# Kernel optimization log

Measured on AMD Instinct MI355X. Metric: run time of the kernel, lower is better.

The kernel has to match this reference:

```python
import jax, jax.numpy as jnp
import numpy as np

B = 4096      # graphs
N = 21        # nodes per graph (EEG electrodes)
CIN = 512
H1 = 1024
H2 = 1024
COUT = 512
R = 4         # SE reduction
RANK = 10     # nodevec rank
EPS = 1e-5
THRESH = 0.1


def setup_inputs() -> dict:
    key = jax.random.key(0)
    ks = jax.random.split(key, 16)
    p = lambda i, shape, s=0.02: (jax.random.normal(ks[i], shape, jnp.float32) * s)
    return {
        "x": jax.random.normal(ks[0], (B * N, CIN), jnp.float32),
        "batch": jnp.arange(B * N, dtype=jnp.int32) // N,
        "nodevec1": jax.random.normal(ks[1], (N, RANK), jnp.float32),
        "nodevec2": jax.random.normal(ks[2], (RANK, N), jnp.float32),
        "se_w1": p(3, (CIN, CIN // R), 0.05),
        "se_w2": p(4, (CIN // R, CIN), 0.05),
        "W1": p(5, (CIN, H1)), "b1": jnp.zeros((H1,), jnp.float32),
        "W2": p(6, (H1, H2)), "b2": jnp.zeros((H2,), jnp.float32),
        "W3": p(7, (H2, COUT)), "b3": jnp.zeros((COUT,), jnp.float32),
        "bn1_g": jnp.ones((H1,), jnp.float32), "bn1_b": jnp.zeros((H1,), jnp.float32),
        "bn2_g": jnp.ones((H2,), jnp.float32), "bn2_b": jnp.zeros((H2,), jnp.float32),
        "bn3_g": jnp.ones((COUT,), jnp.float32), "bn3_b": jnp.zeros((COUT,), jnp.float32),
        "rs1_w": p(8, (CIN, H1)), "rs1_b": jnp.zeros((H1,), jnp.float32),
        "fc_w": p(9, (COUT, 2 * COUT)), "fc_b": jnp.zeros((2 * COUT,), jnp.float32),
    }


def _batchnorm(h, g, b):
    # training-mode BN: biased batch stats over the node dimension
    m = h.mean(0)
    v = h.var(0)
    return (h - m) * jax.lax.rsqrt(v + EPS) * g + b


def _gcn(A, h, W, b):
    # GCNConv with precomputed normalized+thresholded weights:
    # out = A_block_diag @ (h @ W) + b, done densely per graph since A is 21x21
    hm = (h @ W).reshape(B, N, -1)                 # [B, N, Cout]
    agg = jnp.einsum('ij,bjc->bic', A, hm)         # message passing per graph
    return agg.reshape(B * N, -1) + b


def _forward(x, batch, nodevec1, nodevec2, se_w1, se_w2,
             W1, b1, W2, b2, W3, b3,
             bn1_g, bn1_b, bn2_g, bn2_b, bn3_g, bn3_b,
             rs1_w, rs1_b, fc_w, fc_b):
    # SE layer on [B, N, C]: channel-wise gating from node-mean features
    x3 = x.reshape(B, N, CIN)
    y = jax.nn.sigmoid(jax.nn.relu(x3.mean(1) @ se_w1) @ se_w2)   # [B, C]
    xg = (x3 * y[:, None, :]).reshape(B * N, CIN)
    # adaptive adjacency: sigmoid(nv1 @ nv2), symmetric normalize, threshold
    adp = jax.nn.sigmoid(nodevec1 @ nodevec2)                      # [N, N]
    at = adp + jnp.eye(N, dtype=adp.dtype)
    deg = at.sum(1)
    dinv = jnp.where(deg > 0, deg ** -0.5, 0.0)
    A = dinv[:, None] * at * dinv[None, :]
    A = jnp.where(A > THRESH, A, 0.0)
    # layer 1 (+ projected residual, BN, relu; dropout omitted = eval)
    h = _batchnorm(_gcn(A, xg, W1, b1), bn1_g, bn1_b) + (xg @ rs1_w + rs1_b)
    h = jax.nn.relu(h)
    # layer 2 (h1 == h2 -> identity residual)
    h = jax.nn.relu(_batchnorm(_gcn(A, h, W2, b2), bn2_g, bn2_b) + h)
    # layer 3
    h = _batchnorm(_gcn(A, h, W3, b3), bn3_g, bn3_b)
    # global mean pool by graph id
    ssum = jax.ops.segment_sum(h, batch, num_segments=B)
    cnt = jax.ops.segment_sum(jnp.ones((h.shape[0], 1), h.dtype), batch, num_segments=B)
    pooled = ssum / cnt
    return pooled @ fc_w + fc_b                                    # [B, 2*COUT]


def reference(x, batch, nodevec1, nodevec2, se_w1, se_w2,
              W1, b1, W2, b2, W3, b3,
              bn1_g, bn1_b, bn2_g, bn2_b, bn3_g, bn3_b,
              rs1_w, rs1_b, fc_w, fc_b):
    return _forward(x, batch, nodevec1, nodevec2, se_w1, se_w2,
                    W1, b1, W2, b2, W3, b3,
                    bn1_g, bn1_b, bn2_g, bn2_b, bn3_g, bn3_b,
                    rs1_w, rs1_b, fc_w, fc_b)
```

## Files before the change

### kernel.cpp

```cpp
#include <hip/hip_runtime.h>

typedef _Float16 f16;
typedef f16 f16x2 __attribute__((ext_vector_type(2)));
typedef f16 f16x8 __attribute__((ext_vector_type(8)));
typedef float f32x4 __attribute__((ext_vector_type(4)));
typedef const void __attribute__((address_space(1)))* gas1;
typedef void __attribute__((address_space(3)))* las3;

#define NB 4096
#define NN 21
#define MROWS (NB*NN)
#define CIN 512

__global__ void k_adj(const float* __restrict__ nv1, const float* __restrict__ nv2,
                      float* __restrict__ Aout) {
  __shared__ float at[21][21];
  __shared__ float dinv[21];
  int t = threadIdx.x;
  if (t < 441) {
    int i = t / 21, j = t % 21;
    float s = 0.f;
    #pragma unroll
    for (int r = 0; r < 10; r++) s += nv1[i*10 + r] * nv2[r*21 + j];
    float v = 1.f / (1.f + expf(-s));
    if (i == j) v += 1.f;
    at[i][j] = v;
  }
  __syncthreads();
  if (t < 21) {
    float d = 0.f;
    #pragma unroll
    for (int j = 0; j < 21; j++) d += at[t][j];
    dinv[t] = d > 0.f ? rsqrtf(d) : 0.f;
  }
  __syncthreads();
  if (t < 441) {
    int i = t / 21, j = t % 21;
    float a = dinv[i] * at[i][j] * dinv[j];
    Aout[t] = a > 0.1f ? a : 0.f;
  }
}

__global__ void k_transpose(const float* __restrict__ src, f16* __restrict__ dst,
                            int K, int N) {
  __shared__ float tile[32][33];
  int n0 = blockIdx.x * 32, k0 = blockIdx.y * 32;
  int tx = threadIdx.x, ty = threadIdx.y;
  #pragma unroll
  for (int i = 0; i < 4; i++)
    tile[ty + 8*i][tx] = src[(size_t)(k0 + ty + 8*i) * N + n0 + tx];
  __syncthreads();
  #pragma unroll
  for (int i = 0; i < 4; i++)
    dst[(size_t)(n0 + ty + 8*i) * K + k0 + tx] = (f16)tile[tx][ty + 8*i];
}

__global__ void k_mean(const float* __restrict__ x, float* __restrict__ xm) {
  int b = blockIdx.x, t = threadIdx.x;
  for (int c = t; c < CIN; c += 256) {
    float s = 0.f;
    #pragma unroll
    for (int n = 0; n < NN; n++) s += x[((size_t)b*NN + n)*CIN + c];
    xm[(size_t)b*CIN + c] = s * (1.f/21.f);
  }
}

__global__ void k_se1(const float* __restrict__ xm, const float* __restrict__ w1,
                      float* __restrict__ y1) {
  __shared__ float row[CIN];
  int b = blockIdx.x, t = threadIdx.x;
  for (int k = t; k < CIN; k += 128) row[k] = xm[(size_t)b*CIN + k];
  __syncthreads();
  float acc = 0.f;
  for (int k = 0; k < CIN; k++) acc += row[k] * w1[(size_t)k*128 + t];
  y1[(size_t)b*128 + t] = fmaxf(acc, 0.f);
}

__global__ void k_se2(const float* __restrict__ y1, const float* __restrict__ w2,
                      float* __restrict__ y) {
  __shared__ float row[128];
  int b = blockIdx.x, t = threadIdx.x;
  if (t < 128) row[t] = y1[(size_t)b*128 + t];
  __syncthreads();
  float acc = 0.f;
  for (int k = 0; k < 128; k++) acc += row[k] * w2[(size_t)k*CIN + t];
  y[(size_t)b*CIN + t] = 1.f / (1.f + expf(-acc));
}

__global__ void k_gate(const float* __restrict__ x, const float* __restrict__ y,
                       f16* __restrict__ xg) {
  size_t i8 = (size_t)blockIdx.x * 256 + threadIdx.x;
  size_t base = i8 * 8;
  int r = (int)(base >> 9);
  int c = (int)(base & 511);
  int b = r / 21;
  const float4* xp = (const float4*)(x + base);
  const float4* yp = (const float4*)(y + (size_t)b*CIN + c);
  float4 a0 = xp[0], a1 = xp[1];
  float4 g0 = yp[0], g1 = yp[1];
  f16x8 o;
  o[0] = (f16)(a0.x * g0.x); o[1] = (f16)(a0.y * g0.y);
  o[2] = (f16)(a0.z * g0.z); o[3] = (f16)(a0.w * g0.w);
  o[4] = (f16)(a1.x * g1.x); o[5] = (f16)(a1.y * g1.y);
  o[6] = (f16)(a1.z * g1.z); o[7] = (f16)(a1.w * g1.w);
  *(f16x8*)(xg + base) = o;
}

#define GBM 128
#define GBN 128
#define HBUF 32768

template<int MODE>
__global__ __launch_bounds__(256, 2)
void k_gemm4(const f16* __restrict__ A, const f16* __restrict__ BT,
             f16* __restrict__ C1, const float* __restrict__ bias,
             float* __restrict__ Cf, float* __restrict__ psum,
             float* __restrict__ psq, int N, int K, int lgn) {
  __shared__ __align__(16) char lds[2 * HBUF];
  const int tid = threadIdx.x;
  const int nwg = gridDim.x;
  const int g = blockIdx.x;
  const int swz = (g & 7) * (nwg >> 3) + (g >> 3);
  const int bn = swz & ((1 << lgn) - 1);
  const int bm = swz >> lgn;
  const int lane = tid & 63;
  const int wid = tid >> 6;
  const int wr = wid >> 1;
  const int wc = wid & 1;
  const int fr = lane & 15;
  const int kg = lane >> 4;

  size_t srcOff[8]; int ldsOff[8];
  #pragma unroll
  for (int j = 0; j < 8; j++) {
    int gid = j * 256 + tid;
    int row = (gid >> 3) & 127;
    int gr = gid & 7;
    int gsw = gr ^ (row & 7);
    if (gid < 1024) {
      srcOff[j] = (size_t)(bm * GBM + row) * K + gsw * 8;
      ldsOff[j] = gid * 16;
    } else {
      srcOff[j] = (size_t)(bn * GBN + row) * K + gsw * 8;
      ldsOff[j] = 16384 + (gid - 1024) * 16;
    }
  }

  int aOff[4], axor[4], bOff[4], bxor[4];
  #pragma unroll
  for (int m = 0; m < 4; m++) {
    int row = wr*64 + m*16 + fr;
    aOff[m] = row * 128; axor[m] = row & 7;
  }
  #pragma unroll
  for (int n = 0; n < 4; n++) {
    int row = wc*64 + n*16 + fr;
    bOff[n] = 16384 + row * 128; bxor[n] = row & 7;
  }

  f32x4 acc[4][4];
  #pragma unroll
  for (int m = 0; m < 4; m++)
    #pragma unroll
    for (int n = 0; n < 4; n++)
      #pragma unroll
      for (int r = 0; r < 4; r++) acc[m][n][r] = 0.f;

  auto STAGE8 = [&](int t2, int sbuf) {
    char* dst = (char*)lds + sbuf * HBUF;
    const size_t kof = (size_t)t2 * 64;
    #pragma unroll
    for (int j = 0; j < 8; j++) {
      const f16* src = (j < 4 ? A : BT) + srcOff[j] + kof;
      __builtin_amdgcn_global_load_lds((gas1)src, (las3)(dst + ldsOff[j]), 16, 0, 0);
    }
  };
  auto READF = [&](f16x8* avv, f16x8* bvv, const char* rb, int s) {
    #pragma unroll
    for (int m = 0; m < 4; m++)
      avv[m] = *(const f16x8*)(rb + aOff[m] + (((s*4 + kg) ^ axor[m]) << 4));
    #pragma unroll
    for (int n = 0; n < 4; n++)
      bvv[n] = *(const f16x8*)(rb + bOff[n] + (((s*4 + kg) ^ bxor[n]) << 4));
  };

  f16x8 av0[4], bv0[4], av1[4], bv1[4];
  const int NT = K >> 6;
  STAGE8(0, 0);
  asm volatile("s_waitcnt vmcnt(0)" ::: "memory");
  asm volatile("s_barrier" ::: "memory");
  READF(av0, bv0, (const char*)lds, 0);

  for (int t = 0; t < NT; t++) {
    const char* rb  = (const char*)lds + (t & 1) * HBUF;
    const char* rbn = (const char*)lds + ((t + 1) & 1) * HBUF;
    const bool stg = (t + 1) < NT;

    if (stg) STAGE8(t + 1, (t + 1) & 1);
    READF(av1, bv1, rb, 1);
    __builtin_amdgcn_s_setprio(1);
    #pragma unroll
    for (int m = 0; m < 4; m++)
      #pragma unroll
      for (int n = 0; n < 4; n++)
        acc[m][n] = __builtin_amdgcn_mfma_f32_16x16x32_f16(av0[m], bv0[n], acc[m][n], 0, 0, 0);
    __builtin_amdgcn_s_setprio(0);
    if (stg) asm volatile("s_waitcnt vmcnt(0)" ::: "memory");
    asm volatile("s_barrier" ::: "memory");
    if (stg) READF(av0, bv0, rbn, 0);
    __builtin_amdgcn_s_setprio(1);
    #pragma unroll
    for (int m = 0; m < 4; m++)
      #pragma unroll
      for (int n = 0; n < 4; n++)
        acc[m][n] = __builtin_amdgcn_mfma_f32_16x16x32_f16(av1[m], bv1[n], acc[m][n], 0, 0, 0);
    __builtin_amdgcn_s_setprio(0);
  }

  const int crow = bm * GBM + wr * 64 + ((lane >> 4) << 2);
  const int ccol = bn * GBN + wc * 64 + fr;
  if constexpr (MODE == 2) {
    #pragma unroll
    for (int n = 0; n < 4; n++) {
      float bb = bias[ccol + n*16];
      #pragma unroll
      for (int m = 0; m < 4; m++)
        #pragma unroll
        for (int r = 0; r < 4; r++)
          Cf[(size_t)(crow + m*16 + r) * N + (ccol + n*16)] = acc[m][n][r] + bb;
    }
  } else {
    #pragma unroll
    for (int m = 0; m < 4; m++)
      #pragma unroll
      for (int n = 0; n < 4; n++)
        #pragma unroll
        for (int r = 0; r < 4; r++)
          C1[(size_t)(crow + m*16 + r) * N + (ccol + n*16)] = (f16)acc[m][n][r];
  }
  if constexpr (MODE == 1) {
    float s[4], q[4];
    #pragma unroll
    for (int n = 0; n < 4; n++) {
      float ss = 0.f, qq = 0.f;
      #pragma unroll
      for (int m = 0; m < 4; m++)
        #pragma unroll
        for (int r = 0; r < 4; r++) { float v = acc[m][n][r]; ss += v; qq = fmaf(v, v, qq); }
      s[n] = ss; q[n] = qq;
    }
    #pragma unroll
    for (int n = 0; n < 4; n++) {
      s[n] += __shfl_xor(s[n], 16); s[n] += __shfl_xor(s[n], 32);
      q[n] += __shfl_xor(q[n], 16); q[n] += __shfl_xor(q[n], 32);
    }
    float* wred = (float*)lds;
    __syncthreads();
    if ((lane >> 4) == 0) {
      #pragma unroll
      for (int n = 0; n < 4; n++) {
        wred[wr*128 + wc*64 + n*16 + fr]       = s[n];
        wred[256 + wr*128 + wc*64 + n*16 + fr] = q[n];
      }
    }
    __syncthreads();
    if (tid < 128) {
      psum[(size_t)bm * N + bn*128 + tid] = wred[tid]       + wred[128 + tid];
      psq [(size_t)bm * N + bn*128 + tid] = wred[256 + tid] + wred[384 + tid];
    }
  }
}

__global__ __launch_bounds__(256)
void k_mixip(f16* __restrict__ t, const float* __restrict__ Aadj) {
  __shared__ float A[441];
  int b = blockIdx.x, tid = threadIdx.x;
  for (int i = tid; i < 441; i += 256) A[i] = Aadj[i];
  __syncthreads();
  int c0 = tid * 2;
  size_t base = (size_t)b * NN * 512 + c0;
  float vx[21], vy[21];
  #pragma unroll
  for (int j = 0; j < 21; j++) {
    f16x2 v = *(const f16x2*)(t + base + (size_t)j * 512);
    vx[j] = (float)v[0]; vy[j] = (float)v[1];
  }
  #pragma unroll
  for (int i = 0; i < 21; i++) {
    float a0 = 0.f, a1 = 0.f;
    #pragma unroll
    for (int j = 0; j < 21; j++) { float w = A[i*21+j]; a0 = fmaf(w, vx[j], a0); a1 = fmaf(w, vy[j], a1); }
    f16x2 o; o[0] = (f16)a0; o[1] = (f16)a1;
    *(f16x2*)(t + base + (size_t)i * 512) = o;
  }
}

__global__ __launch_bounds__(256)
void k_mix(f16* __restrict__ t, const float* __restrict__ Aadj,
           float* __restrict__ psum, float* __restrict__ psq, int C) {
  __shared__ float A[441];
  int b = blockIdx.x, tid = threadIdx.x;
  for (int i = tid; i < 441; i += 256) A[i] = Aadj[i];
  __syncthreads();
  int c0 = (blockIdx.y * 256 + tid) * 2;
  size_t base = (size_t)b * NN * C + c0;
  float vx[21], vy[21];
  #pragma unroll
  for (int j = 0; j < 21; j++) {
    f16x2 v = *(const f16x2*)(t + base + (size_t)j * C);
    vx[j] = (float)v[0]; vy[j] = (float)v[1];
  }
  float s0 = 0.f, s1 = 0.f, q0 = 0.f, q1 = 0.f;
  #pragma unroll
  for (int i = 0; i < 21; i++) {
    float a0 = 0.f, a1 = 0.f;
    #pragma unroll
    for (int j = 0; j < 21; j++) {
      float w = A[i*21 + j];
      a0 = fmaf(w, vx[j], a0);
      a1 = fmaf(w, vy[j], a1);
    }
    f16x2 o; o[0] = (f16)a0; o[1] = (f16)a1;
    *(f16x2*)(t + base + (size_t)i * C) = o;
    s0 += a0; s1 += a1;
    q0 = fmaf(a0, a0, q0); q1 = fmaf(a1, a1, q1);
  }
  float2 sv; sv.x = s0; sv.y = s1;
  float2 qv; qv.x = q0; qv.y = q1;
  *(float2*)(psum + (size_t)b * C + c0) = sv;
  *(float2*)(psq  + (size_t)b * C + c0) = qv;
}

__global__ void k_reduce(const float* __restrict__ ps, const float* __restrict__ pq,
                         float* __restrict__ rs, float* __restrict__ rq,
                         int C, int per) {
  int c = blockIdx.x * 256 + threadIdx.x;
  int py = blockIdx.y;
  float s = 0.f, q = 0.f;
  for (int p = py*per; p < py*per + per; p++) {
    s += ps[(size_t)p*C + c];
    q += pq[(size_t)p*C + c];
  }
  rs[(size_t)py*C + c] = s;
  rq[(size_t)py*C + c] = q;
}

__global__ void k_bnparams(const float* __restrict__ psum, const float* __restrict__ psq,
                           const float* __restrict__ gamma, const float* __restrict__ beta,
                           const float* __restrict__ resbias,
                           float* __restrict__ scale, float* __restrict__ shift,
                           int C, int npart) {
  int c = blockIdx.x * 256 + threadIdx.x;
  float s = 0.f, q = 0.f;
  for (int p = 0; p < npart; p++) { s += psum[(size_t)p*C + c]; q += psq[(size_t)p*C + c]; }
  const float Minv = 1.f / (float)MROWS;
  float mean = s * Minv;
  float var = q * Minv - mean * mean;
  float sc = gamma[c] * rsqrtf(var + 1e-5f);
  float sh = beta[c] - mean * sc;
  if (resbias) sh += resbias[c];
  scale[c] = sc; shift[c] = sh;
}

__global__ void k_finalize(const f16* __restrict__ g, const f16* res,
                           f16* dst, const float* __restrict__ scale,
                           const float* __restrict__ shift, int cmask) {
  size_t i8 = (size_t)blockIdx.x * 256 + threadIdx.x;
  size_t base = i8 * 8;
  int c = (int)(base & (size_t)cmask);
  f16x8 gv = *(const f16x8*)(g + base);
  f16x8 rv = *(const f16x8*)(res + base);
  f16x8 o;
  #pragma unroll
  for (int j = 0; j < 8; j++) {
    float v = (float)gv[j] * scale[c + j] + shift[c + j] + (float)rv[j];
    o[j] = (f16)fmaxf(v, 0.f);
  }
  *(f16x8*)(dst + base) = o;
}

__global__ __launch_bounds__(256)
void k_finmix(const f16* t, const f16* res, f16* hout, f16* hmix,
              const float* __restrict__ scale, const float* __restrict__ shift,
              const float* __restrict__ Aadj, int C) {
  __shared__ float A[441];
  int b = blockIdx.x, tid = threadIdx.x;
  for (int i = tid; i < 441; i += 256) A[i] = Aadj[i];
  __syncthreads();
  int c0 = (blockIdx.y * 256 + tid) * 2;
  float scx = scale[c0], scy = scale[c0+1];
  float shx = shift[c0], shy = shift[c0+1];
  size_t base = (size_t)b * NN * C + c0;
  float hx[21], hy[21];
  #pragma unroll
  for (int j = 0; j < 21; j++) {
    f16x2 tv = *(const f16x2*)(t + base + (size_t)j*C);
    f16x2 rv = *(const f16x2*)(res + base + (size_t)j*C);
    hx[j] = fmaxf((float)tv[0]*scx + shx + (float)rv[0], 0.f);
    hy[j] = fmaxf((float)tv[1]*scy + shy + (float)rv[1], 0.f);
    if (hout) {
      f16x2 o; o[0] = (f16)hx[j]; o[1] = (f16)hy[j];
      *(f16x2*)(hout + base + (size_t)j*C) = o;
    }
  }
  #pragma unroll
  for (int i = 0; i < 21; i++) {
    float a0 = 0.f, a1 = 0.f;
    #pragma unroll
    for (int j = 0; j < 21; j++) { float w = A[i*21+j]; a0 = fmaf(w, hx[j], a0); a1 = fmaf(w, hy[j], a1); }
    f16x2 o; o[0] = (f16)a0; o[1] = (f16)a1;
    *(f16x2*)(hmix + base + (size_t)i*C) = o;
  }
}

__global__ void k_pool(const f16* __restrict__ g3, const float* __restrict__ scale,
                       const float* __restrict__ shift, f16* __restrict__ pooled) {
  int b = blockIdx.x, t = threadIdx.x;
  for (int c = t; c < 512; c += 256) {
    float s = 0.f;
    #pragma unroll
    for (int n = 0; n < NN; n++) s += (float)g3[((size_t)b*NN + n)*512 + c];
    pooled[(size_t)b*512 + c] = (f16)((s * (1.f/21.f)) * scale[c] + shift[c]);
  }
}

extern "C" void kernel_launch(void* const* d_in, const int* in_sizes, int n_in,
                              void* d_out, int out_size, void* d_ws, size_t ws_size,
                              hipStream_t stream) {
  const float* x     = (const float*)d_in[0];
  const float* nv1   = (const float*)d_in[2];
  const float* nv2   = (const float*)d_in[3];
  const float* se_w1 = (const float*)d_in[4];
  const float* se_w2 = (const float*)d_in[5];
  const float* W1    = (const float*)d_in[6];
  const float* W2    = (const float*)d_in[8];
  const float* W3    = (const float*)d_in[10];
  const float* bn1g  = (const float*)d_in[12];
  const float* bn1b  = (const float*)d_in[13];
  const float* bn2g  = (const float*)d_in[14];
  const float* bn2b  = (const float*)d_in[15];
  const float* bn3g  = (const float*)d_in[16];
  const float* bn3b  = (const float*)d_in[17];
  const float* rs1w  = (const float*)d_in[18];
  const float* rs1b  = (const float*)d_in[19];
  const float* fcw   = (const float*)d_in[20];
  const float* fcb   = (const float*)d_in[21];
  float* out = (float*)d_out;

  char* ws = (char*)d_ws;
  size_t off = 0;
  auto alloc = [&](size_t bytes) -> char* {
    char* p = ws + off;
    off = (off + bytes + 255) & ~(size_t)255;
    return p;
  };

  float* A_adj = (float*)alloc(441 * 4);
  f16* W1T  = (f16*)alloc((size_t)1024 * 512 * 2);
  f16* RS1T = (f16*)alloc((size_t)1024 * 512 * 2);
  f16* W2T  = (f16*)alloc((size_t)1024 * 1024 * 2);
  f16* W3T  = (f16*)alloc((size_t)512 * 1024 * 2);
  f16* FCWT = (f16*)alloc((size_t)1024 * 512 * 2);
  float* psum = (float*)alloc((size_t)NB * 1024 * 4);
  float* psq  = (float*)alloc((size_t)NB * 1024 * 4);
  float* y1   = (float*)alloc((size_t)NB * 128 * 4);
  float* rsum = (float*)alloc((size_t)32 * 1024 * 4);
  float* rsq  = (float*)alloc((size_t)32 * 1024 * 4);
  float* sc1 = (float*)alloc(1024 * 4);
  float* sh1 = (float*)alloc(1024 * 4);
  float* sc2 = (float*)alloc(1024 * 4);
  float* sh2 = (float*)alloc(1024 * 4);
  float* sc3 = (float*)alloc(1024 * 4);
  float* sh3 = (float*)alloc(1024 * 4);
  f16* pooled = (f16*)alloc((size_t)NB * 512 * 2);
  f16* G = (f16*)alloc((size_t)MROWS * 512 * 2);
  f16* R = (f16*)alloc((size_t)MROWS * 1024 * 2);
  f16* T = (f16*)alloc((size_t)MROWS * 1024 * 2);
  float* xm = psum;
  float* yv = psq;
  (void)ws_size; (void)in_sizes; (void)n_in; (void)out_size;

  k_adj<<<1, 512, 0, stream>>>(nv1, nv2, A_adj);
  k_transpose<<<dim3(32, 16), dim3(32, 8), 0, stream>>>(W1,   W1T,  512, 1024);
  k_transpose<<<dim3(32, 16), dim3(32, 8), 0, stream>>>(rs1w, RS1T, 512, 1024);
  k_transpose<<<dim3(32, 32), dim3(32, 8), 0, stream>>>(W2,   W2T,  1024, 1024);
  k_transpose<<<dim3(16, 32), dim3(32, 8), 0, stream>>>(W3,   W3T,  1024, 512);
  k_transpose<<<dim3(32, 16), dim3(32, 8), 0, stream>>>(fcw,  FCWT, 512, 1024);

  k_mean<<<NB, 256, 0, stream>>>(x, xm);
  k_se1<<<NB, 128, 0, stream>>>(xm, se_w1, y1);
  k_se2<<<NB, 512, 0, stream>>>(y1, se_w2, yv);
  k_gate<<<21504, 256, 0, stream>>>(x, yv, G);

  k_gemm4<0><<<672*8, 256, 0, stream>>>(G, RS1T, R, nullptr, nullptr, nullptr, nullptr, 1024, 512, 3);
  k_mixip<<<NB, 256, 0, stream>>>(G, A_adj);
  k_gemm4<1><<<672*8, 256, 0, stream>>>(G, W1T, T, nullptr, nullptr, psum, psq, 1024, 512, 3);
  k_reduce<<<dim3(4, 32), 256, 0, stream>>>(psum, psq, rsum, rsq, 1024, 21);
  k_bnparams<<<4, 256, 0, stream>>>(rsum, rsq, bn1g, bn1b, rs1b, sc1, sh1, 1024, 32);
  k_finalize<<<43008, 256, 0, stream>>>(T, R, R, sc1, sh1, 1023);

  k_gemm4<0><<<672*8, 256, 0, stream>>>(R, W2T, T, nullptr, nullptr, nullptr, nullptr, 1024, 1024, 3);
  k_mix<<<dim3(NB, 2), 256, 0, stream>>>(T, A_adj, psum, psq, 1024);
  k_reduce<<<dim3(4, 32), 256, 0, stream>>>(psum, psq, rsum, rsq, 1024, 128);
  k_bnparams<<<4, 256, 0, stream>>>(rsum, rsq, bn2g, bn2b, nullptr, sc2, sh2, 1024, 32);
  k_finmix<<<dim3(NB, 2), 256, 0, stream>>>(T, R, nullptr, T, sc2, sh2, A_adj, 1024);

  k_gemm4<1><<<672*4, 256, 0, stream>>>(T, W3T, G, nullptr, nullptr, psum, psq, 512, 1024, 2);
  k_reduce<<<dim3(2, 32), 256, 0, stream>>>(psum, psq, rsum, rsq, 512, 21);
  k_bnparams<<<2, 256, 0, stream>>>(rsum, rsq, bn3g, bn3b, nullptr, sc3, sh3, 512, 32);

  k_pool<<<NB, 256, 0, stream>>>(G, sc3, sh3, pooled);
  k_gemm4<2><<<32*8, 256, 0, stream>>>(pooled, FCWT, nullptr, fcb, out, nullptr, nullptr, 1024, 512, 3);
}
```

Before: 1.214 ms.

## Switch GEMMs to 256x256 tiles with 512 threads and vectorized epilogue

Replaces the 128x128, 256-thread GEMM with a 256x256, 512-thread (8-wave) kernel using 128 KB of double-buffered LDS. Global-to-LDS staging is split into halves interleaved with the two MFMA sub-steps, and operands are swapped so each lane owns four contiguous output columns, allowing f16x4 and float4 stores. The goals are higher arithmetic intensity per LDS byte, fewer global loads per FLOP and wider stores. In exchange, occupancy drops to one workgroup per CU and register pressure rises. The BN partial-sum layout and the reduce/bnparams launch counts change to match the new row-block count.

```diff
diff --git a/kernel.cpp b/kernel.cpp
--- a/kernel.cpp
+++ b/kernel.cpp
@@ -2,6 +2,7 @@
 
 typedef _Float16 f16;
 typedef f16 f16x2 __attribute__((ext_vector_type(2)));
+typedef f16 f16x4 __attribute__((ext_vector_type(4)));
 typedef f16 f16x8 __attribute__((ext_vector_type(8)));
 typedef float f32x4 __attribute__((ext_vector_type(4)));
 typedef const void __attribute__((address_space(1)))* gas1;
@@ -106,17 +107,15 @@
   *(f16x8*)(xg + base) = o;
 }
 
-#define GBM 128
-#define GBN 128
-#define HBUF 32768
+#define QBUF 65536
 
 template<int MODE>
-__global__ __launch_bounds__(256, 2)
-void k_gemm4(const f16* __restrict__ A, const f16* __restrict__ BT,
-             f16* __restrict__ C1, const float* __restrict__ bias,
-             float* __restrict__ Cf, float* __restrict__ psum,
-             float* __restrict__ psq, int N, int K, int lgn) {
-  __shared__ __align__(16) char lds[2 * HBUF];
+__global__ __launch_bounds__(512, 1)
+void k_gemm256(const f16* __restrict__ A, const f16* __restrict__ BT,
+               f16* __restrict__ C1, const float* __restrict__ bias,
+               float* __restrict__ Cf, float* __restrict__ psum,
+               float* __restrict__ psq, int N, int K, int lgn) {
+  __shared__ __align__(16) char lds[2 * QBUF];
   const int tid = threadIdx.x;
   const int nwg = gridDim.x;
   const int g = blockIdx.x;
@@ -125,148 +124,145 @@
   const int bm = swz >> lgn;
   const int lane = tid & 63;
   const int wid = tid >> 6;
-  const int wr = wid >> 1;
-  const int wc = wid & 1;
+  const int wr = wid >> 2;
+  const int wc = wid & 3;
   const int fr = lane & 15;
   const int kg = lane >> 4;
 
-  size_t srcOff[8]; int ldsOff[8];
+  int srcOff[8];
   #pragma unroll
   for (int j = 0; j < 8; j++) {
-    int gid = j * 256 + tid;
-    int row = (gid >> 3) & 127;
+    int gid = j * 512 + tid;
+    int row = (gid >> 3) & 255;
     int gr = gid & 7;
     int gsw = gr ^ (row & 7);
-    if (gid < 1024) {
-      srcOff[j] = (size_t)(bm * GBM + row) * K + gsw * 8;
-      ldsOff[j] = gid * 16;
-    } else {
-      srcOff[j] = (size_t)(bn * GBN + row) * K + gsw * 8;
-      ldsOff[j] = 16384 + (gid - 1024) * 16;
-    }
-  }
-
-  int aOff[4], axor[4], bOff[4], bxor[4];
-  #pragma unroll
-  for (int m = 0; m < 4; m++) {
-    int row = wr*64 + m*16 + fr;
-    aOff[m] = row * 128; axor[m] = row & 7;
-  }
-  #pragma unroll
-  for (int n = 0; n < 4; n++) {
-    int row = wc*64 + n*16 + fr;
-    bOff[n] = 16384 + row * 128; bxor[n] = row & 7;
-  }
-
-  f32x4 acc[4][4];
-  #pragma unroll
-  for (int m = 0; m < 4; m++)
+    srcOff[j] = ((j < 4 ? bm : bn) * 256 + row) * K + gsw * 8;
+  }
+  const int ldsBase = tid * 16;
+
+  const int x7 = fr & 7;
+  const int aBase = (wr*128 + fr) * 128;
+  const int bBase = 32768 + (wc*64 + fr) * 128;
+
+  f32x4 acc[8][4];
+  #pragma unroll
+  for (int m = 0; m < 8; m++)
     #pragma unroll
     for (int n = 0; n < 4; n++)
       #pragma unroll
       for (int r = 0; r < 4; r++) acc[m][n][r] = 0.f;
 
-  auto STAGE8 = [&](int t2, int sbuf) {
-    char* dst = (char*)lds + sbuf * HBUF;
+  auto STAGEH = [&](int t2, int sbuf, int j0) {
+    char* dst = (char*)lds + sbuf * QBUF;
     const size_t kof = (size_t)t2 * 64;
     #pragma unroll
-    for (int j = 0; j < 8; j++) {
+    for (int j = j0; j < j0 + 2; j++) {
       const f16* src = (j < 4 ? A : BT) + srcOff[j] + kof;
-      __builtin_amdgcn_global_load_lds((gas1)src, (las3)(dst + ldsOff[j]), 16, 0, 0);
+      __builtin_amdgcn_global_load_lds((gas1)src, (las3)(dst + ldsBase + j*8192), 16, 0, 0);
     }
   };
-  auto READF = [&](f16x8* avv, f16x8* bvv, const char* rb, int s) {
-    #pragma unroll
-    for (int m = 0; m < 4; m++)
-      avv[m] = *(const f16x8*)(rb + aOff[m] + (((s*4 + kg) ^ axor[m]) << 4));
-    #pragma unroll
-    for (int n = 0; n < 4; n++)
-      bvv[n] = *(const f16x8*)(rb + bOff[n] + (((s*4 + kg) ^ bxor[n]) << 4));
+  auto READF = [&](f16x8* av, f16x8* bv, const char* rb, int s) {
+    const int ko = ((s*4 + kg) ^ x7) << 4;
+    #pragma unroll
+    for (int m = 0; m < 8; m++) av[m] = *(const f16x8*)(rb + aBase + m*2048 + ko);
+    #pragma unroll
+    for (int n = 0; n < 4; n++) bv[n] = *(const f16x8*)(rb + bBase + n*2048 + ko);
   };
 
-  f16x8 av0[4], bv0[4], av1[4], bv1[4];
+  f16x8 av[8], bv[4];
   const int NT = K >> 6;
-  STAGE8(0, 0);
+  STAGEH(0, 0, 0); STAGEH(0, 0, 2); STAGEH(0, 0, 4); STAGEH(0, 0, 6);
   asm volatile("s_waitcnt vmcnt(0)" ::: "memory");
   asm volatile("s_barrier" ::: "memory");
-  READF(av0, bv0, (const char*)lds, 0);
 
   for (int t = 0; t < NT; t++) {
-    const char* rb  = (const char*)lds + (t & 1) * HBUF;
-    const char* rbn = (const char*)lds + ((t + 1) & 1) * HBUF;
+    const char* rb = (const char*)lds + (t & 1) * QBUF;
+    const int nb = (t + 1) & 1;
     const bool stg = (t + 1) < NT;
 
-    if (stg) STAGE8(t + 1, (t + 1) & 1);
-    READF(av1, bv1, rb, 1);
+    if (stg) { STAGEH(t + 1, nb, 0); STAGEH(t + 1, nb, 2); }
+    READF(av, bv, rb, 0);
     __builtin_amdgcn_s_setprio(1);
     #pragma unroll
-    for (int m = 0; m < 4; m++)
+    for (int m = 0; m < 8; m++)
       #pragma unroll
       for (int n = 0; n < 4; n++)
-        acc[m][n] = __builtin_amdgcn_mfma_f32_16x16x32_f16(av0[m], bv0[n], acc[m][n], 0, 0, 0);
+        acc[m][n] = __builtin_amdgcn_mfma_f32_16x16x32_f16(bv[n], av[m], acc[m][n], 0, 0, 0);
+    __builtin_amdgcn_s_setprio(0);
+    if (stg) { STAGEH(t + 1, nb, 4); STAGEH(t + 1, nb, 6); }
+    READF(av, bv, rb, 1);
+    __builtin_amdgcn_s_setprio(1);
+    #pragma unroll
+    for (int m = 0; m < 8; m++)
+      #pragma unroll
+      for (int n = 0; n < 4; n++)
+        acc[m][n] = __builtin_amdgcn_mfma_f32_16x16x32_f16(bv[n], av[m], acc[m][n], 0, 0, 0);
     __builtin_amdgcn_s_setprio(0);
     if (stg) asm volatile("s_waitcnt vmcnt(0)" ::: "memory");
     asm volatile("s_barrier" ::: "memory");
-    if (stg) READF(av0, bv0, rbn, 0);
-    __builtin_amdgcn_s_setprio(1);
-    #pragma unroll
-    for (int m = 0; m < 4; m++)
-      #pragma unroll
-      for (int n = 0; n < 4; n++)
-        acc[m][n] = __builtin_amdgcn_mfma_f32_16x16x32_f16(av1[m], bv1[n], acc[m][n], 0, 0, 0);
-    __builtin_amdgcn_s_setprio(0);
-  }
-
-  const int crow = bm * GBM + wr * 64 + ((lane >> 4) << 2);
-  const int ccol = bn * GBN + wc * 64 + fr;
+  }
+
+  const int crow = bm*256 + wr*128 + fr;
+  const int ccol = bn*256 + wc*64 + kg*4;
   if constexpr (MODE == 2) {
     #pragma unroll
     for (int n = 0; n < 4; n++) {
-      float bb = bias[ccol + n*16];
-      #pragma unroll
-      for (int m = 0; m < 4; m++)
-        #pragma unroll
-        for (int r = 0; r < 4; r++)
-          Cf[(size_t)(crow + m*16 + r) * N + (ccol + n*16)] = acc[m][n][r] + bb;
+      float4 bb = *(const float4*)(bias + ccol + n*16);
+      #pragma unroll
+      for (int m = 0; m < 8; m++) {
+        float4 v;
+        v.x = acc[m][n][0] + bb.x; v.y = acc[m][n][1] + bb.y;
+        v.z = acc[m][n][2] + bb.z; v.w = acc[m][n][3] + bb.w;
+        *(float4*)(Cf + (size_t)(crow + m*16) * N + ccol + n*16) = v;
+      }
     }
   } else {
     #pragma unroll
-    for (int m = 0; m < 4; m++)
+    for (int m = 0; m < 8; m++)
+      #pragma unroll
+      for (int n = 0; n < 4; n++) {
+        f16x4 o;
+        o[0] = (f16)acc[m][n][0]; o[1] = (f16)acc[m][n][1];
+        o[2] = (f16)acc[m][n][2]; o[3] = (f16)acc[m][n][3];
+        *(f16x4*)(C1 + (size_t)(crow + m*16) * N + ccol + n*16) = o;
+      }
+  }
+  if constexpr (MODE == 1) {
+    float s[4][4], q[4][4];
+    #pragma unroll
+    for (int n = 0; n < 4; n++)
+      #pragma unroll
+      for (int r = 0; r < 4; r++) {
+        float ss = 0.f, qq = 0.f;
+        #pragma unroll
+        for (int m = 0; m < 8; m++) { float v = acc[m][n][r]; ss += v; qq = fmaf(v, v, qq); }
+        s[n][r] = ss; q[n][r] = qq;
+      }
+    #pragma unroll
+    for (int n = 0; n < 4; n++)
+      #pragma unroll
+      for (int r = 0; r < 4; r++) {
+        s[n][r] += __shfl_xor(s[n][r], 1); s[n][r] += __shfl_xor(s[n][r], 2);
+        s[n][r] += __shfl_xor(s[n][r], 4); s[n][r] += __shfl_xor(s[n][r], 8);
+        q[n][r] += __shfl_xor(q[n][r], 1); q[n][r] += __shfl_xor(q[n][r], 2);
+        q[n][r] += __shfl_xor(q[n][r], 4); q[n][r] += __shfl_xor(q[n][r], 8);
+      }
+    float* wred = (float*)lds;
+    __syncthreads();
+    if (fr == 0) {
       #pragma unroll
       for (int n = 0; n < 4; n++)
         #pragma unroll
-        for (int r = 0; r < 4; r++)
-          C1[(size_t)(crow + m*16 + r) * N + (ccol + n*16)] = (f16)acc[m][n][r];
-  }
-  if constexpr (MODE == 1) {
-    float s[4], q[4];
-    #pragma unroll
-    for (int n = 0; n < 4; n++) {
-      float ss = 0.f, qq = 0.f;
-      #pragma unroll
-      for (int m = 0; m < 4; m++)
-        #pragma unroll
-        for (int r = 0; r < 4; r++) { float v = acc[m][n][r]; ss += v; qq = fmaf(v, v, qq); }
-      s[n] = ss; q[n] = qq;
-    }
-    #pragma unroll
-    for (int n = 0; n < 4; n++) {
-      s[n] += __shfl_xor(s[n], 16); s[n] += __shfl_xor(s[n], 32);
-      q[n] += __shfl_xor(q[n], 16); q[n] += __shfl_xor(q[n], 32);
-    }
-    float* wred = (float*)lds;
-    __syncthreads();
-    if ((lane >> 4) == 0) {
-      #pragma unroll
-      for (int n = 0; n < 4; n++) {
-        wred[wr*128 + wc*64 + n*16 + fr]       = s[n];
-        wred[256 + wr*128 + wc*64 + n*16 + fr] = q[n];
-      }
+        for (int r = 0; r < 4; r++) {
+          int c = wc*64 + n*16 + kg*4 + r;
+          wred[wr*256 + c]       = s[n][r];
+          wred[512 + wr*256 + c] = q[n][r];
+        }
     }
     __syncthreads();
-    if (tid < 128) {
-      psum[(size_t)bm * N + bn*128 + tid] = wred[tid]       + wred[128 + tid];
-      psq [(size_t)bm * N + bn*128 + tid] = wred[256 + tid] + wred[384 + tid];
+    if (tid < 256) {
+      psum[(size_t)bm * N + bn*256 + tid] = wred[tid]       + wred[256 + tid];
+      psq [(size_t)bm * N + bn*256 + tid] = wred[512 + tid] + wred[768 + tid];
     }
   }
 }
@@ -492,23 +488,23 @@
   k_se2<<<NB, 512, 0, stream>>>(y1, se_w2, yv);
   k_gate<<<21504, 256, 0, stream>>>(x, yv, G);
 
-  k_gemm4<0><<<672*8, 256, 0, stream>>>(G, RS1T, R, nullptr, nullptr, nullptr, nullptr, 1024, 512, 3);
+  k_gemm256<0><<<1344, 512, 0, stream>>>(G, RS1T, R, nullptr, nullptr, nullptr, nullptr, 1024, 512, 2);
   k_mixip<<<NB, 256, 0, stream>>>(G, A_adj);
-  k_gemm4<1><<<672*8, 256, 0, stream>>>(G, W1T, T, nullptr, nullptr, psum, psq, 1024, 512, 3);
-  k_reduce<<<dim3(4, 32), 256, 0, stream>>>(psum, psq, rsum, rsq, 1024, 21);
-  k_bnparams<<<4, 256, 0, stream>>>(rsum, rsq, bn1g, bn1b, rs1b, sc1, sh1, 1024, 32);
+  k_gemm256<1><<<1344, 512, 0, stream>>>(G, W1T, T, nullptr, nullptr, psum, psq, 1024, 512, 2);
+  k_reduce<<<dim3(4, 24), 256, 0, stream>>>(psum, psq, rsum, rsq, 1024, 14);
+  k_bnparams<<<4, 256, 0, stream>>>(rsum, rsq, bn1g, bn1b, rs1b, sc1, sh1, 1024, 24);
   k_finalize<<<43008, 256, 0, stream>>>(T, R, R, sc1, sh1, 1023);
 
-  k_gemm4<0><<<672*8, 256, 0, stream>>>(R, W2T, T, nullptr, nullptr, nullptr, nullptr, 1024, 1024, 3);
+  k_gemm256<0><<<1344, 512, 0, stream>>>(R, W2T, T, nullptr, nullptr, nullptr, nullptr, 1024, 1024, 2);
   k_mix<<<dim3(NB, 2), 256, 0, stream>>>(T, A_adj, psum, psq, 1024);
   k_reduce<<<dim3(4, 32), 256, 0, stream>>>(psum, psq, rsum, rsq, 1024, 128);
   k_bnparams<<<4, 256, 0, stream>>>(rsum, rsq, bn2g, bn2b, nullptr, sc2, sh2, 1024, 32);
   k_finmix<<<dim3(NB, 2), 256, 0, stream>>>(T, R, nullptr, T, sc2, sh2, A_adj, 1024);
 
-  k_gemm4<1><<<672*4, 256, 0, stream>>>(T, W3T, G, nullptr, nullptr, psum, psq, 512, 1024, 2);
-  k_reduce<<<dim3(2, 32), 256, 0, stream>>>(psum, psq, rsum, rsq, 512, 21);
-  k_bnparams<<<2, 256, 0, stream>>>(rsum, rsq, bn3g, bn3b, nullptr, sc3, sh3, 512, 32);
+  k_gemm256<1><<<672, 512, 0, stream>>>(T, W3T, G, nullptr, nullptr, psum, psq, 512, 1024, 1);
+  k_reduce<<<dim3(2, 24), 256, 0, stream>>>(psum, psq, rsum, rsq, 512, 14);
+  k_bnparams<<<2, 256, 0, stream>>>(rsum, rsq, bn3g, bn3b, nullptr, sc3, sh3, 512, 24);
 
   k_pool<<<NB, 256, 0, stream>>>(G, sc3, sh3, pooled);
-  k_gemm4<2><<<32*8, 256, 0, stream>>>(pooled, FCWT, nullptr, fcb, out, nullptr, nullptr, 1024, 512, 3);
-}
+  k_gemm256<2><<<64, 512, 0, stream>>>(pooled, FCWT, nullptr, fcb, out, nullptr, nullptr, 1024, 512, 2);
+}
```

Measured after the change: 1.180 ms. -2.8%, faster.
